# Optimization experiments

Hardware: AMD Instinct MI355X
Metric: run time of the kernel (lower is better)

## Reference

```python
import jax, jax.numpy as jnp
import numpy as np

B, S, D_MODEL, D_HEAD = 4, 4096, 768, 64

def setup_inputs() -> dict:
    key = jax.random.key(0)
    kx, kq, kk, kv = jax.random.split(key, 4)
    scale = 1.0 / np.sqrt(D_MODEL)
    return {
        "x": jax.random.normal(kx, (B, S, D_MODEL), dtype=jnp.float32),
        "W_Q": jax.random.normal(kq, (D_MODEL, D_HEAD), dtype=jnp.float32) * scale,
        "W_K": jax.random.normal(kk, (D_MODEL, D_HEAD), dtype=jnp.float32) * scale,
        "W_V": jax.random.normal(kv, (D_MODEL, D_HEAD), dtype=jnp.float32) * scale,
    }

def reference(x, W_Q, W_K, W_V):
    # x: [B, S, d_model]; projections to [B, S, d_head]
    Q = x @ W_Q
    K = x @ W_K
    V = x @ W_V
    d_head = Q.shape[-1]
    # scores: [B, S, S], scaled dot product
    A = jnp.einsum('bid,bjd->bij', Q, K) / jnp.sqrt(jnp.asarray(d_head, Q.dtype))
    S_len = x.shape[1]
    causal = jnp.tril(jnp.ones((S_len, S_len), dtype=bool))
    A = jnp.where(causal[None, :, :], A, -jnp.inf)
    A = jax.nn.softmax(A, axis=-1)
    return jnp.einsum('bij,bjd->bid', A, V)
```

## Files before the change

### kernel.cpp

```cpp
#include <hip/hip_runtime.h>
#include <hip/hip_bf16.h>

typedef __bf16 bf16_t;
typedef bf16_t bf16x8 __attribute__((ext_vector_type(8)));
typedef float f32x4 __attribute__((ext_vector_type(4)));
typedef float f32x16 __attribute__((ext_vector_type(16)));
typedef unsigned int u32;

#define NB 4
#define SS 4096
#define DM 768
#define DH 64
#define NROW (NB * SS)
#define CSCALE (0.125f * 1.44269504088896341f)
#define MFIX 24.0f

#define QOFF 0u
#define KOFF 2097152u
#define VOFF 4194304u
#define WOFF 6291456u

#define SB() __builtin_amdgcn_sched_barrier(0)

__device__ __forceinline__ u32 cvtpk_bf16(float lo, float hi) {
    u32 r;
    asm volatile("v_cvt_pk_bf16_f32 %0, %1, %2" : "=v"(r) : "v"(lo), "v"(hi));
    return r;
}

__global__ __launch_bounds__(256) void wt_kernel(const float* __restrict__ wq,
                                                 const float* __restrict__ wk,
                                                 const float* __restrict__ wv,
                                                 bf16_t* __restrict__ wt) {
    int id = blockIdx.x * 256 + threadIdx.x;
    if (id >= 3 * DM * DH) return;
    int m = id / (DM * DH);
    int r = id - m * (DM * DH);
    int k = r >> 6;
    int c = r & 63;
    const float* w = (m == 0) ? wq : (m == 1) ? wk : wv;
    wt[(size_t)m * DH * DM + (size_t)c * DM + k] = (bf16_t)w[k * DH + c];
}

__global__ __launch_bounds__(256, 4) void proj_kernel(const float* __restrict__ x,
                                                      const bf16_t* __restrict__ wt,
                                                      bf16_t* __restrict__ Qo,
                                                      bf16_t* __restrict__ Ko,
                                                      bf16_t* __restrict__ Vt) {
    __shared__ __align__(16) float xs[2][1024];

    const int tid = threadIdx.x;
    const int lane = tid & 63;
    const int wid = tid >> 6;
    const int l15 = lane & 15;
    const int g = lane >> 4;
    const int m0 = blockIdx.x * 16;

    const int srow = tid >> 4;
    const int skc = (tid & 15) ^ (srow & 7);
    const float* sbase = x + (size_t)(m0 + srow) * DM + skc * 4;

    #define STAGE(bsel, t_)                                                         \
        __builtin_amdgcn_global_load_lds(                                           \
            (const __attribute__((address_space(1))) void*)(sbase + (t_) * 64),     \
            (__attribute__((address_space(3))) void*)(&xs[bsel][wid * 256]),        \
            16, 0, 0);

    size_t wbase[3];
    #pragma unroll
    for (int n = 0; n < 3; n++) {
        const int gn = wid * 3 + n;
        const int mm = gn >> 2;
        const int cj = gn & 3;
        wbase[n] = (size_t)mm * DH * DM + (size_t)(cj * 16 + l15) * DM + g * 8;
    }

    f32x4 acc[3];
    #pragma unroll
    for (int n = 0; n < 3; n++)
        #pragma unroll
        for (int j = 0; j < 4; j++) acc[n][j] = 0.0f;

    int roff[2][2];
    #pragma unroll
    for (int kk = 0; kk < 2; kk++)
        #pragma unroll
        for (int c = 0; c < 2; c++)
            roff[kk][c] = l15 * 64 + ((kk * 8 + g * 2 + c) ^ (l15 & 7)) * 4;

    STAGE(0, 0);
    bf16x8 wcur[3][2], wnext[3][2];
    #pragma unroll
    for (int n = 0; n < 3; n++)
        #pragma unroll
        for (int kk = 0; kk < 2; kk++)
            wcur[n][kk] = *reinterpret_cast<const bf16x8*>(wt + wbase[n] + kk * 32);
    __syncthreads();

    #pragma unroll
    for (int t = 0; t < 12; t++) {
        const int cur = t & 1;
        if (t < 11) {
            STAGE(cur ^ 1, t + 1);
            #pragma unroll
            for (int n = 0; n < 3; n++)
                #pragma unroll
                for (int kk = 0; kk < 2; kk++)
                    wnext[n][kk] = *reinterpret_cast<const bf16x8*>(
                        wt + wbase[n] + (t + 1) * 64 + kk * 32);
        }
        bf16x8 a[2];
        #pragma unroll
        for (int kk = 0; kk < 2; kk++) {
            f32x4 c0 = *reinterpret_cast<const f32x4*>(&xs[cur][roff[kk][0]]);
            f32x4 c1 = *reinterpret_cast<const f32x4*>(&xs[cur][roff[kk][1]]);
            bf16x8 tt;
            #pragma unroll
            for (int j = 0; j < 4; j++) { tt[j] = (bf16_t)c0[j]; tt[4 + j] = (bf16_t)c1[j]; }
            a[kk] = tt;
        }
        #pragma unroll
        for (int n = 0; n < 3; n++)
            #pragma unroll
            for (int kk = 0; kk < 2; kk++)
                acc[n] = __builtin_amdgcn_mfma_f32_16x16x32_bf16(a[kk], wcur[n][kk], acc[n], 0, 0, 0);

        if (t < 11) {
            __syncthreads();
            #pragma unroll
            for (int n = 0; n < 3; n++)
                #pragma unroll
                for (int kk = 0; kk < 2; kk++)
                    wcur[n][kk] = wnext[n][kk];
        }
    }
    #undef STAGE

    #pragma unroll
    for (int n = 0; n < 3; n++) {
        const int gn = wid * 3 + n;
        const int mm = gn >> 2;
        const int cj = gn & 3;
        #pragma unroll
        for (int j = 0; j < 4; j++) {
            int row = m0 + g * 4 + j;
            int col = cj * 16 + l15;
            float v = acc[n][j];
            if (mm == 0)      Qo[(size_t)row * DH + col] = (bf16_t)(v * CSCALE);
            else if (mm == 1) Ko[(size_t)row * DH + col] = (bf16_t)v;
            else              Vt[(size_t)col * NROW + row] = (bf16_t)v;
        }
    }
}

__global__ __launch_bounds__(256, 2) void attn_kernel(const bf16_t* __restrict__ Q,
                                                      const bf16_t* __restrict__ K,
                                                      const bf16_t* __restrict__ Vt,
                                                      float* __restrict__ out) {
    __shared__ float Ob[2][2][16][64];
    __shared__ float Ls[2][64];

    const int tid = threadIdx.x;
    const int lane = tid & 63;
    const int w = tid >> 6;
    const int l31 = lane & 31;
    const int hi = lane >> 5;
    const int bx = blockIdx.x;
    const int b = (bx & 7) >> 1;
    const int r_ = (bx >> 3) * 2 + (bx & 1);
    const int tile = (r_ < 64) ? (127 - r_) : (r_ - 64);
    const int q0 = tile * 32;
    const int nkv = (tile >> 1) + 1;
    const int q = q0 + l31;

    const bf16_t* Qb = Q + (size_t)b * SS * DH;
    const bf16_t* Kb = K + (size_t)b * SS * DH;
    const bf16_t* Vb = Vt + (size_t)b * SS;

    bf16x8 bq[4];
    #pragma unroll
    for (int ks = 0; ks < 4; ks++)
        bq[ks] = *reinterpret_cast<const bf16x8*>(
            Qb + (size_t)(q0 + l31) * DH + ks * 16 + hi * 8);

    f32x16 o[2];
    #pragma unroll
    for (int c = 0; c < 2; c++)
        #pragma unroll
        for (int r = 0; r < 16; r++) o[c][r] = 0.0f;
    float lsum = 0.0f;

    for (int kt = w; kt < nkv; kt += 4) {
        const int kv0 = kt * 64;
        const bool diag = (kv0 + 63 > q0);

        bf16x8 ak0[4];
        #pragma unroll
        for (int ks = 0; ks < 4; ks++)
            ak0[ks] = *reinterpret_cast<const bf16x8*>(
                Kb + (size_t)(kv0 + l31) * DH + ks * 16 + hi * 8);
        SB();
        bf16x8 ak1[4];
        #pragma unroll
        for (int ks = 0; ks < 4; ks++)
            ak1[ks] = *reinterpret_cast<const bf16x8*>(
                Kb + (size_t)(kv0 + 32 + l31) * DH + ks * 16 + hi * 8);
        SB();
        bf16x8 vf[2][4];
        #pragma unroll
        for (int c = 0; c < 2; c++)
            #pragma unroll
            for (int kks = 0; kks < 4; kks++)
                vf[c][kks] = *reinterpret_cast<const bf16x8*>(
                    Vb + (size_t)(c * 32 + l31) * NROW + kv0 + kks * 16 + hi * 8);
        SB();

        u32 pa[4][4];
        f32x16 s0;
        #pragma unroll
        for (int r = 0; r < 16; r++) s0[r] = 0.0f;
        #pragma unroll
        for (int ks = 0; ks < 4; ks++)
            s0 = __builtin_amdgcn_mfma_f32_32x32x16_bf16(ak0[ks], bq[ks], s0, 0, 0, 0);
        f32x16 s1;
        #pragma unroll
        for (int r = 0; r < 16; r++) s1[r] = 0.0f;
        #pragma unroll
        for (int ks = 0; ks < 4; ks++)
            s1 = __builtin_amdgcn_mfma_f32_32x32x16_bf16(ak1[ks], bq[ks], s1, 0, 0, 0);

        #pragma unroll
        for (int blk = 0; blk < 2; blk++) {
            const f32x16& s = blk ? s1 : s0;
            const int kvbase = kv0 + blk * 32 + 4 * hi;
            float p[16];
            #pragma unroll
            for (int r = 0; r < 16; r++) {
                float e = exp2f(s[r] - MFIX);
                if (diag) {
                    int kv = kvbase + (r & 3) + 8 * (r >> 2);
                    e = (kv > q) ? 0.0f : e;
                }
                p[r] = e;
                lsum += e;
            }
            #pragma unroll
            for (int ks2 = 0; ks2 < 2; ks2++) {
                u32 w01 = cvtpk_bf16(p[8 * ks2 + 0], p[8 * ks2 + 1]);
                u32 w23 = cvtpk_bf16(p[8 * ks2 + 2], p[8 * ks2 + 3]);
                u32 w45 = cvtpk_bf16(p[8 * ks2 + 4], p[8 * ks2 + 5]);
                u32 w67 = cvtpk_bf16(p[8 * ks2 + 6], p[8 * ks2 + 7]);
                asm volatile("v_permlane32_swap_b32 %0, %1" : "+v"(w01), "+v"(w45));
                asm volatile("v_permlane32_swap_b32 %0, %1" : "+v"(w23), "+v"(w67));
                pa[blk * 2 + ks2][0] = w01;
                pa[blk * 2 + ks2][1] = w23;
                pa[blk * 2 + ks2][2] = w45;
                pa[blk * 2 + ks2][3] = w67;
            }
        }

        #pragma unroll
        for (int kks = 0; kks < 4; kks++) {
            union { u32 w4[4]; bf16x8 v; } uu;
            uu.w4[0] = pa[kks][0];
            uu.w4[1] = pa[kks][1];
            uu.w4[2] = pa[kks][2];
            uu.w4[3] = pa[kks][3];
            #pragma unroll
            for (int c = 0; c < 2; c++)
                o[c] = __builtin_amdgcn_mfma_f32_32x32x16_bf16(uu.v, vf[c][kks], o[c], 0, 0, 0);
        }
    }

    if (w >= 2) {
        #pragma unroll
        for (int c = 0; c < 2; c++)
            #pragma unroll
            for (int r = 0; r < 16; r++) Ob[w - 2][c][r][lane] = o[c][r];
        Ls[w - 2][lane] = lsum;
    }
    __syncthreads();
    if (w < 2) {
        #pragma unroll
        for (int c = 0; c < 2; c++)
            #pragma unroll
            for (int r = 0; r < 16; r++) o[c][r] += Ob[w][c][r][lane];
        lsum += Ls[w][lane];
    }
    __syncthreads();
    if (w == 1) {
        #pragma unroll
        for (int c = 0; c < 2; c++)
            #pragma unroll
            for (int r = 0; r < 16; r++) Ob[0][c][r][lane] = o[c][r];
        Ls[0][lane] = lsum;
    }
    __syncthreads();
    if (w == 0) {
        #pragma unroll
        for (int c = 0; c < 2; c++)
            #pragma unroll
            for (int r = 0; r < 16; r++) o[c][r] += Ob[0][c][r][lane];
        lsum += Ls[0][lane];

        float lfull = lsum + __shfl_xor(lsum, 32);
        float* ob = out + ((size_t)b * SS + q0) * DH;
        #pragma unroll
        for (int c = 0; c < 2; c++)
            #pragma unroll
            for (int r = 0; r < 16; r++) {
                const int qr = (r & 3) + 8 * (r >> 2) + 4 * hi;
                float lr = __shfl(lfull, qr);
                ob[(size_t)qr * DH + c * 32 + l31] = o[c][r] / lr;
            }
    }
}

extern "C" void kernel_launch(void* const* d_in, const int* in_sizes, int n_in,
                              void* d_out, int out_size, void* d_ws, size_t ws_size,
                              hipStream_t stream) {
    const float* x  = (const float*)d_in[0];
    const float* wq = (const float*)d_in[1];
    const float* wk = (const float*)d_in[2];
    const float* wv = (const float*)d_in[3];
    float* out = (float*)d_out;

    char* ws = (char*)d_ws;
    bf16_t* Qw = (bf16_t*)(ws + QOFF);
    bf16_t* Kw = (bf16_t*)(ws + KOFF);
    bf16_t* Vt = (bf16_t*)(ws + VOFF);
    bf16_t* Wt = (bf16_t*)(ws + WOFF);

    hipLaunchKernelGGL(wt_kernel, dim3((3 * DM * DH + 255) / 256), dim3(256), 0, stream,
                       wq, wk, wv, Wt);
    hipLaunchKernelGGL(proj_kernel, dim3(NROW / 16), dim3(256), 0, stream,
                       x, Wt, Qw, Kw, Vt);
    hipLaunchKernelGGL(attn_kernel, dim3(NB * 128), dim3(256), 0, stream,
                       Qw, Kw, Vt, out);
}
```

Before: 82.91 us.

## Deepen projection pipeline to four LDS stages with 512-thread 32-row tiles

The projection kernel now processes 32 rows per block with 8 waves, sharing the staged x tile across two row-halves. The x stage goes from a double buffer to a four-deep LDS ring, and the weight registers from two slots to a three-slot rotation. Explicit vmcnt waits and raw barriers replace __syncthreads so more loads stay in flight. The aim is to hide global-load latency in the projection. In exchange the block uses more LDS and registers, occupancy may drop, and the hand-tuned waitcnt counts are fragile.

```diff
diff --git a/kernel.cpp b/kernel.cpp
--- a/kernel.cpp
+++ b/kernel.cpp
@@ -42,19 +42,21 @@
     wt[(size_t)m * DH * DM + (size_t)c * DM + k] = (bf16_t)w[k * DH + c];
 }
 
-__global__ __launch_bounds__(256, 4) void proj_kernel(const float* __restrict__ x,
+__global__ __launch_bounds__(512, 4) void proj_kernel(const float* __restrict__ x,
                                                       const bf16_t* __restrict__ wt,
                                                       bf16_t* __restrict__ Qo,
                                                       bf16_t* __restrict__ Ko,
                                                       bf16_t* __restrict__ Vt) {
-    __shared__ __align__(16) float xs[2][1024];
+    __shared__ __align__(16) float xs[4][2048];
 
     const int tid = threadIdx.x;
     const int lane = tid & 63;
     const int wid = tid >> 6;
+    const int wr = wid & 1;
+    const int wc = wid >> 1;
     const int l15 = lane & 15;
     const int g = lane >> 4;
-    const int m0 = blockIdx.x * 16;
+    const int m0 = blockIdx.x * 32;
 
     const int srow = tid >> 4;
     const int skc = (tid & 15) ^ (srow & 7);
@@ -69,7 +71,7 @@
     size_t wbase[3];
     #pragma unroll
     for (int n = 0; n < 3; n++) {
-        const int gn = wid * 3 + n;
+        const int gn = wc * 3 + n;
         const int mm = gn >> 2;
         const int cj = gn & 3;
         wbase[n] = (size_t)mm * DH * DM + (size_t)(cj * 16 + l15) * DM + g * 8;
@@ -81,39 +83,54 @@
         #pragma unroll
         for (int j = 0; j < 4; j++) acc[n][j] = 0.0f;
 
+    const int arow = wr * 16 + l15;
     int roff[2][2];
     #pragma unroll
     for (int kk = 0; kk < 2; kk++)
         #pragma unroll
         for (int c = 0; c < 2; c++)
-            roff[kk][c] = l15 * 64 + ((kk * 8 + g * 2 + c) ^ (l15 & 7)) * 4;
-
-    STAGE(0, 0);
-    bf16x8 wcur[3][2], wnext[3][2];
+            roff[kk][c] = arow * 64 + ((kk * 8 + g * 2 + c) ^ (arow & 7)) * 4;
+
+    bf16x8 wslot[3][3][2];
+
     #pragma unroll
     for (int n = 0; n < 3; n++)
         #pragma unroll
         for (int kk = 0; kk < 2; kk++)
-            wcur[n][kk] = *reinterpret_cast<const bf16x8*>(wt + wbase[n] + kk * 32);
-    __syncthreads();
+            wslot[0][n][kk] = *reinterpret_cast<const bf16x8*>(wt + wbase[n] + kk * 32);
+    SB();
+    STAGE(0, 0); SB();
+    #pragma unroll
+    for (int n = 0; n < 3; n++)
+        #pragma unroll
+        for (int kk = 0; kk < 2; kk++)
+            wslot[1][n][kk] = *reinterpret_cast<const bf16x8*>(wt + wbase[n] + 64 + kk * 32);
+    SB();
+    STAGE(1, 1); SB();
+    STAGE(2, 2); SB();
+    asm volatile("s_waitcnt vmcnt(8)");
+    SB();
+    __builtin_amdgcn_s_barrier();
+    SB();
 
     #pragma unroll
     for (int t = 0; t < 12; t++) {
-        const int cur = t & 1;
-        if (t < 11) {
-            STAGE(cur ^ 1, t + 1);
+        if (t + 2 < 12) {
             #pragma unroll
             for (int n = 0; n < 3; n++)
                 #pragma unroll
                 for (int kk = 0; kk < 2; kk++)
-                    wnext[n][kk] = *reinterpret_cast<const bf16x8*>(
-                        wt + wbase[n] + (t + 1) * 64 + kk * 32);
-        }
+                    wslot[(t + 2) % 3][n][kk] = *reinterpret_cast<const bf16x8*>(
+                        wt + wbase[n] + (t + 2) * 64 + kk * 32);
+        }
+        SB();
+        if (t + 3 < 12) { STAGE((t + 3) & 3, t + 3); }
+        SB();
         bf16x8 a[2];
         #pragma unroll
         for (int kk = 0; kk < 2; kk++) {
-            f32x4 c0 = *reinterpret_cast<const f32x4*>(&xs[cur][roff[kk][0]]);
-            f32x4 c1 = *reinterpret_cast<const f32x4*>(&xs[cur][roff[kk][1]]);
+            f32x4 c0 = *reinterpret_cast<const f32x4*>(&xs[t & 3][roff[kk][0]]);
+            f32x4 c1 = *reinterpret_cast<const f32x4*>(&xs[t & 3][roff[kk][1]]);
             bf16x8 tt;
             #pragma unroll
             for (int j = 0; j < 4; j++) { tt[j] = (bf16_t)c0[j]; tt[4 + j] = (bf16_t)c1[j]; }
@@ -123,27 +140,27 @@
         for (int n = 0; n < 3; n++)
             #pragma unroll
             for (int kk = 0; kk < 2; kk++)
-                acc[n] = __builtin_amdgcn_mfma_f32_16x16x32_bf16(a[kk], wcur[n][kk], acc[n], 0, 0, 0);
+                acc[n] = __builtin_amdgcn_mfma_f32_16x16x32_bf16(a[kk], wslot[t % 3][n][kk], acc[n], 0, 0, 0);
 
         if (t < 11) {
-            __syncthreads();
-            #pragma unroll
-            for (int n = 0; n < 3; n++)
-                #pragma unroll
-                for (int kk = 0; kk < 2; kk++)
-                    wcur[n][kk] = wnext[n][kk];
+            if (t <= 8)       { asm volatile("s_waitcnt vmcnt(8)"); }
+            else if (t == 9)  { asm volatile("s_waitcnt vmcnt(7)"); }
+            else              { asm volatile("s_waitcnt vmcnt(0)"); }
+            SB();
+            __builtin_amdgcn_s_barrier();
+            SB();
         }
     }
     #undef STAGE
 
     #pragma unroll
     for (int n = 0; n < 3; n++) {
-        const int gn = wid * 3 + n;
+        const int gn = wc * 3 + n;
         const int mm = gn >> 2;
         const int cj = gn & 3;
         #pragma unroll
         for (int j = 0; j < 4; j++) {
-            int row = m0 + g * 4 + j;
+            int row = m0 + wr * 16 + g * 4 + j;
             int col = cj * 16 + l15;
             float v = acc[n][j];
             if (mm == 0)      Qo[(size_t)row * DH + col] = (bf16_t)(v * CSCALE);
@@ -333,7 +350,7 @@
 
     hipLaunchKernelGGL(wt_kernel, dim3((3 * DM * DH + 255) / 256), dim3(256), 0, stream,
                        wq, wk, wv, Wt);
-    hipLaunchKernelGGL(proj_kernel, dim3(NROW / 16), dim3(256), 0, stream,
+    hipLaunchKernelGGL(proj_kernel, dim3(NROW / 32), dim3(512), 0, stream,
                        x, Wt, Qw, Kw, Vt);
     hipLaunchKernelGGL(attn_kernel, dim3(NB * 128), dim3(256), 0, stream,
                        Qw, Kw, Vt, out);
```

Measured after the change: 81.68 us. About the same (-1.5%).
